# Optimization experiments

Hardware: AMD Instinct MI355X
Metric: run time of the kernel (lower is better)

## Reference

```python
import jax, jax.numpy as jnp
import numpy as np

B, N, DPOS, F, P, K = 32, 1024, 3, 64, 128, 16


def setup_inputs() -> dict:
    key = jax.random.key(0)
    kp, kf, kw1, kw2 = jax.random.split(key, 4)
    points = jax.random.normal(kp, (B, N, DPOS), dtype=jnp.float32)
    features = jax.random.normal(kf, (B, N, F), dtype=jnp.float32)
    W1 = jax.random.normal(kw1, (2 * F, 2 * P), dtype=jnp.float32) * (1.0 / np.sqrt(2 * F))
    b1 = jnp.zeros((2 * P,), dtype=jnp.float32)
    W2 = jax.random.normal(kw2, (2 * P, P), dtype=jnp.float32) * (1.0 / np.sqrt(2 * P))
    b2 = jnp.zeros((P,), dtype=jnp.float32)
    return {"points": points, "features": features, "W1": W1, "b1": b1, "W2": W2, "b2": b2}


def reference(points, features, W1, b1, W2, b2):
    # pairwise squared distances: r_i - 2 p_i.p_j + r_j + 1e-5  -> [B, N, N]
    r = jnp.sum(points * points, axis=2, keepdims=True)
    m = jnp.einsum('bnd,bmd->bnm', points, points)
    D = r - 2.0 * m + jnp.swapaxes(r, 1, 2) + 1e-5
    # K+1 nearest (incl. self), drop self -> indices [B, N, K]
    _, idx = jax.lax.top_k(-D, K + 1)
    idx = idx[:, :, 1:]
    # gather neighbor features: [B, N, K, F]
    neighbors = features[jnp.arange(B)[:, None, None], idx]
    center = jnp.broadcast_to(features[:, :, None, :], neighbors.shape)
    local = jnp.concatenate([neighbors - center, center], axis=-1)  # [B,N,K,2F]
    # 2-layer MLP with exact GELU
    h = jax.nn.gelu(jnp.einsum('bnkf,fh->bnkh', local, W1) + b1, approximate=False)
    out = jax.nn.gelu(jnp.einsum('bnkh,hp->bnkp', h, W2) + b2, approximate=False)
    # mean over neighbors -> [B, N, P]
    return jnp.mean(out, axis=2)
```

## Files before the change

kernel.cpp:

```cpp
#include <hip/hip_runtime.h>
#include <math.h>

#define BB 32
#define NN 1024
#define FF 64
#define PP 128
#define KNN 16
#define H2 256
#define F2 128
#define KSEL 17
#define SVCAP 272

typedef float f32x4 __attribute__((ext_vector_type(4)));
typedef _Float16 f16x8 __attribute__((ext_vector_type(8)));
typedef _Float16 f16x4 __attribute__((ext_vector_type(4)));
typedef _Float16 f16x2 __attribute__((ext_vector_type(2)));

#define GC1 0.39616247f
#define GC3 -0.05891477f
#define GC5 0.00563735f
#define GC7 -2.10439e-4f
#define GXC 3.2988f

__device__ __forceinline__ f16x8 splat8(float f) {
    _Float16 h = (_Float16)f;
    f16x8 v = {h, h, h, h, h, h, h, h};
    return v;
}
__device__ __forceinline__ f16x4 splat4(float f) {
    _Float16 h = (_Float16)f;
    f16x4 v = {h, h, h, h};
    return v;
}

__device__ __forceinline__ f16x8 act8(f16x8 gv, f16x8 qv) {
    const f16x8 XL = splat8(-GXC), XH = splat8(GXC);
    const f16x8 C1 = splat8(GC1), C3 = splat8(GC3), C5 = splat8(GC5), C7 = splat8(GC7);
    const f16x8 HF = splat8(0.5f);
    f16x8 x  = gv + qv;
    f16x8 xc = __builtin_elementwise_min(__builtin_elementwise_max(x, XL), XH);
    f16x8 s  = xc * xc;
    f16x8 t  = s * C7 + C5;
    t = s * t + C3;
    t = s * t + C1;
    f16x8 u = xc * t + HF;
    return x * u;
}

__device__ __forceinline__ float gelu4_sum(f32x4 a, float bias) {
    f16x4 x;
    x[0] = (_Float16)(a[0] + bias);
    x[1] = (_Float16)(a[1] + bias);
    x[2] = (_Float16)(a[2] + bias);
    x[3] = (_Float16)(a[3] + bias);
    const f16x4 XL = splat4(-GXC), XH = splat4(GXC);
    const f16x4 C1 = splat4(GC1), C3 = splat4(GC3), C5 = splat4(GC5), C7 = splat4(GC7);
    const f16x4 HF = splat4(0.5f);
    f16x4 xc = __builtin_elementwise_min(__builtin_elementwise_max(x, XL), XH);
    f16x4 s  = xc * xc;
    f16x4 t  = s * C7 + C5;
    t = s * t + C3;
    t = s * t + C1;
    f16x4 u = xc * t + HF;
    f16x4 y = x * u;
    f16x2 y2 = __builtin_shufflevector(y, y, 0, 1) + __builtin_shufflevector(y, y, 2, 3);
    return (float)y2[0] + (float)y2[1];
}

template <int OFF>
__device__ __forceinline__ f16x8 gload(const char* a) {
    f16x8 d;
    asm volatile("global_load_dwordx4 %0, %1, off offset:%c2"
                 : "=v"(d) : "v"(a), "i"(OFF));
    return d;
}
template <int N>
__device__ __forceinline__ void vwait() {
    asm volatile("s_waitcnt vmcnt(%c0)" ::"i"(N) : "memory");
    __builtin_amdgcn_sched_barrier(0);
}

__global__ __launch_bounds__(512) void prep_weights(const float* __restrict__ W1,
                                                    const float* __restrict__ W2,
                                                    _Float16* __restrict__ Wcf,
                                                    _Float16* __restrict__ W2f) {
    int tid = blockIdx.x * 512 + threadIdx.x;
    if (tid < 4096) {
        const int lane = tid & 63, quad = lane >> 4, l16 = lane & 15;
        const int kk = (tid >> 6) & 1, n_tile = tid >> 7;
        const int n = n_tile * 16 + l16;
        const int kb = kk * 32 + quad * 8;
        f16x8 v;
#pragma unroll
        for (int j = 0; j < 8; ++j) {
            const int k = kb + j;
            float x = (n < 256) ? W1[k * 256 + n]
                                : (W1[(64 + k) * 256 + (n - 256)] - W1[k * 256 + (n - 256)]);
            v[j] = (_Float16)x;
        }
        *(f16x8*)(Wcf + (size_t)tid * 8) = v;
    } else {
        const int t2 = tid - 4096;
        const int lane = t2 & 63, quad = lane >> 4, l16 = lane & 15;
        const int nt = (t2 >> 6) & 7, kk8 = t2 >> 9;
        const int p = nt * 16 + l16;
        const int hb = kk8 * 32 + quad * 8;
        f16x8 v;
#pragma unroll
        for (int j = 0; j < 8; ++j) v[j] = (_Float16)W2[(size_t)(hb + j) * PP + p];
        *(f16x8*)(W2f + (size_t)t2 * 8) = v;
    }
}

__global__ __launch_bounds__(512, 8) void knn_gq(const float* __restrict__ points,
                                                 int* __restrict__ idx_out,
                                                 const float* __restrict__ feat,
                                                 const _Float16* __restrict__ Wcf,
                                                 const float* __restrict__ b1,
                                                 _Float16* __restrict__ Gall,
                                                 _Float16* __restrict__ Qall) {
    __shared__ __align__(16) unsigned char smem[35840];
    const int t = threadIdx.x;

    if (blockIdx.x >= 4096) {
        _Float16 (*st)[16][136] = (_Float16(*)[16][136])smem;
        const int w8 = t >> 6, lane = t & 63;
        const int w4 = w8 & 3;
        const int quad = lane >> 4, l16 = lane & 15;
        const int gb = blockIdx.x - 4096;
        const int m0 = gb * 32 + (w8 >> 2) * 16;

        f16x8 a[2];
#pragma unroll
        for (int kk = 0; kk < 2; ++kk) {
            const float* ap = feat + (size_t)(m0 + l16) * 64 + kk * 32 + quad * 8;
            float4 a0 = *(const float4*)ap, a1 = *(const float4*)(ap + 4);
            f16x8 v;
            v[0] = (_Float16)a0.x; v[1] = (_Float16)a0.y; v[2] = (_Float16)a0.z; v[3] = (_Float16)a0.w;
            v[4] = (_Float16)a1.x; v[5] = (_Float16)a1.y; v[6] = (_Float16)a1.z; v[7] = (_Float16)a1.w;
            a[kk] = v;
        }
        f32x4 acc[8];
#pragma unroll
        for (int nt = 0; nt < 8; ++nt) acc[nt] = (f32x4){0.f, 0.f, 0.f, 0.f};
#pragma unroll
        for (int kk = 0; kk < 2; ++kk)
#pragma unroll
            for (int nt = 0; nt < 8; ++nt) {
                f16x8 bf = *(const f16x8*)(Wcf + (size_t)(((w4 * 8 + nt) * 2 + kk) * 64 + lane) * 8);
                acc[nt] = __builtin_amdgcn_mfma_f32_16x16x32_f16(a[kk], bf, acc[nt], 0, 0, 0);
            }

        const bool isQ = (w4 >= 2);
#pragma unroll
        for (int nt = 0; nt < 8; ++nt) {
            const int col = nt * 16 + l16;
            const float bias = isQ ? b1[(w4 - 2) * 128 + col] : 0.f;
#pragma unroll
            for (int r = 0; r < 4; ++r)
                st[w8][quad * 4 + r][col] = (_Float16)(acc[nt][r] + bias);
        }
        __syncthreads();

        const int row = lane >> 2, c = lane & 3;
        const int m = m0 + row;
#pragma unroll
        for (int i = 0; i < 4; ++i) {
            const int col = c * 32 + i * 8;
            f16x8 v = *(const f16x8*)&st[w8][row][col];
            if (!isQ) *(f16x8*)(Gall + (size_t)m * H2 + w4 * 128 + col) = v;
            else      *(f16x8*)(Qall + (size_t)m * H2 + (w4 - 2) * 128 + col) = v;
        }
        return;
    }

    float2* pxy = (float2*)smem;
    float2* pzr = (float2*)(smem + 8192);
    unsigned (*sv_val)[SVCAP] = (unsigned(*)[SVCAP])(smem + 16384);
    unsigned (*sv_idx)[SVCAP] = (unsigned(*)[SVCAP])(smem + 25088);
    unsigned (*tie_idx)[64]   = (unsigned(*)[64])(smem + 33792);

    const int w = t >> 6, lane = t & 63;
    const int b = blockIdx.x >> 7;
    const int q0 = (blockIdx.x & 127) * 8;
    const float* pb = points + (size_t)b * NN * 3;
    const unsigned long long lt = (1ull << lane) - 1ull;

    for (int i = t; i < NN; i += 512) {
        float x = pb[3 * i], y = pb[3 * i + 1], z = pb[3 * i + 2];
        float r = __fadd_rn(__fadd_rn(__fmul_rn(x, x), __fmul_rn(y, y)), __fmul_rn(z, z));
        pxy[i] = make_float2(x, y);
        pzr[i] = make_float2(z, r);
    }
    __syncthreads();

    const int qn = q0 + w;
    const int gq = b * NN + qn;
    const float2 qv1 = pxy[qn], qv2 = pzr[qn];
    const float qx = qv1.x, qy = qv1.y, qz = qv2.x, qw = qv2.y;

    float D[16];
#pragma unroll
    for (int j = 0; j < 16; ++j) {
        const int m = j * 64 + lane;
        const float2 v1 = pxy[m], v2 = pzr[m];
        float dot = __fadd_rn(__fadd_rn(__fmul_rn(qx, v1.x), __fmul_rn(qy, v1.y)),
                              __fmul_rn(qz, v2.x));
        D[j] = __fadd_rn(__fadd_rn(__fsub_rn(qw, __fmul_rn(2.0f, dot)), v2.y), 1e-5f);
    }

    float mnf = D[0];
#pragma unroll
    for (int j = 1; j < 16; ++j) mnf = fminf(mnf, D[j]);
    const unsigned mbits = __float_as_uint(mnf);

    const unsigned mhi = mbits >> 16;
    unsigned Thi = 0;
#pragma unroll
    for (int bit = 15; bit >= 0; --bit) {
        unsigned cand = Thi | (1u << bit);
        int cnt = __popcll(__ballot(mhi < cand));
        if (cnt < KSEL) Thi = cand;
    }
    const unsigned T = (Thi << 16) | 0xFFFFu;

    unsigned base = 0;
#pragma unroll
    for (int j = 0; j < 16; ++j) {
        unsigned vb = __float_as_uint(D[j]);
        bool keep = (vb <= T);
        unsigned long long m = __ballot(keep);
        if (keep) {
            unsigned pos = base + (unsigned)__popcll(m & lt);
            if (pos < SVCAP) { sv_val[w][pos] = vb; sv_idx[w][pos] = j * 64 + lane; }
        }
        base += (unsigned)__popcll(m);
    }
    unsigned C = base > SVCAP ? SVCAP : base;

    unsigned rv[5], ri[5];
#pragma unroll
    for (int s = 0; s < 5; ++s) {
        int i = s * 64 + lane;
        bool ok = (i < (int)C);
        rv[s] = ok ? sv_val[w][i] : 0xFFFFFFFFu;
        ri[s] = ok ? sv_idx[w][i] : 0xFFFFFFFFu;
    }

    unsigned Ts = 0;
    if (C <= 64) {
#pragma unroll
        for (int bit = 31; bit >= 0; --bit) {
            unsigned cand = Ts | (1u << bit);
            int cnt = __popcll(__ballot(rv[0] < cand));
            if (cnt < KSEL) Ts = cand;
        }
    } else {
#pragma unroll
        for (int bit = 31; bit >= 0; --bit) {
            unsigned cand = Ts | (1u << bit);
            int cnt = 0;
#pragma unroll
            for (int s = 0; s < 5; ++s)
                cnt += __popcll(__ballot(rv[s] < cand));
            if (cnt < KSEL) Ts = cand;
        }
    }

    int L = 0;
#pragma unroll
    for (int s = 0; s < 5; ++s) L += __popcll(__ballot(rv[s] < Ts));
    const int need = KSEL - L;

    unsigned vmin_l = 0xFFFFFFFFu;
#pragma unroll
    for (int s = 0; s < 5; ++s) vmin_l = vmin_l < rv[s] ? vmin_l : rv[s];
#pragma unroll
    for (int off = 32; off >= 1; off >>= 1) {
        unsigned o2 = __shfl_xor(vmin_l, off, 64);
        vmin_l = vmin_l < o2 ? vmin_l : o2;
    }
    const unsigned Vmin = vmin_l;
    unsigned imin_l = 0xFFFFFFFFu;
#pragma unroll
    for (int s = 0; s < 5; ++s)
        if (rv[s] == Vmin && ri[s] < imin_l) imin_l = ri[s];
#pragma unroll
    for (int off = 32; off >= 1; off >>= 1) {
        unsigned o2 = __shfl_xor(imin_l, off, 64);
        imin_l = imin_l < o2 ? imin_l : o2;
    }
    const unsigned dropIdx = imin_l;

    int* o = idx_out + (size_t)gq * KNN;
    unsigned wbase = 0, tbase = 0;
#pragma unroll
    for (int s = 0; s < 5; ++s) {
        unsigned vb = rv[s], mi = ri[s];
        bool wk = (vb < Ts) && (mi != dropIdx);
        unsigned long long wm = __ballot(wk);
        if (wk) o[wbase + (unsigned)__popcll(wm & lt)] = (int)mi;
        wbase += (unsigned)__popcll(wm);
        bool tk = (vb == Ts);
        unsigned long long tm2 = __ballot(tk);
        if (tk) {
            unsigned tp = tbase + (unsigned)__popcll(tm2 & lt);
            if (tp < 64) tie_idx[w][tp] = mi;
        }
        tbase += (unsigned)__popcll(tm2);
    }
    unsigned tc = tbase > 64 ? 64 : tbase;
    if ((int)tc == need) {
        bool tk = (lane < (int)tc);
        unsigned mi2 = tk ? tie_idx[w][lane] : 0xFFFFFFFFu;
        tk = tk && (mi2 != dropIdx);
        unsigned long long m3 = __ballot(tk);
        if (tk) o[wbase + (unsigned)__popcll(m3 & lt)] = (int)mi2;
    } else if (lane == 0) {
        unsigned pos = wbase;
        for (int r = 0; r < need; ++r) {
            unsigned best = 0xFFFFFFFFu; int bj = 0;
            for (int j2 = 0; j2 < (int)tc; ++j2) {
                unsigned mi = tie_idx[w][j2];
                if (mi < best) { best = mi; bj = j2; }
            }
            tie_idx[w][bj] = 0xFFFFFFFFu;
            if (best != dropIdx) o[pos++] = (int)best;
        }
    }
}

__global__ __launch_bounds__(512, 3) void fused_mlp14(const _Float16* __restrict__ Gall,
                                                      const _Float16* __restrict__ Qall,
                                                      const int* __restrict__ knn_idx,
                                                      const _Float16* __restrict__ W2f,
                                                      const float* __restrict__ b2,
                                                      float* __restrict__ out) {
    __shared__ __align__(16) _Float16 w2s[32768];
    const int t = threadIdx.x, w = t >> 6, lane = t & 63;
    const int quad = lane >> 4, l16 = lane & 15;

    const int lb = ((blockIdx.x & 7) << 8) | (blockIdx.x >> 3);

    const int q0 = lb * 16 + w * 2;
    const int b = q0 >> 10;
    const int nb0 = knn_idx[q0 * KNN + l16];
    const int nb1 = knn_idx[(q0 + 1) * KNN + l16];
    const _Float16* g0 = Gall + ((size_t)(b << 10) + nb0) * H2;
    const _Float16* g1 = Gall + ((size_t)(b << 10) + nb1) * H2;
    const _Float16* qq0 = Qall + (size_t)q0 * H2;
    const _Float16* qq1 = qq0 + H2;

    const char* aG0 = (const char*)g0 + quad * 16;
    const char* aG1 = (const char*)g1 + quad * 16;
    const char* aQ0 = (const char*)qq0 + quad * 16;
    const char* aQ1 = (const char*)qq1 + quad * 16;

    float bias[8];
#pragma unroll
    for (int nt = 0; nt < 8; ++nt) bias[nt] = b2[nt * 16 + l16];
#pragma unroll
    for (int nt = 0; nt < 8; ++nt) asm volatile("" ::"v"(bias[nt]));

#pragma unroll
    for (int i = 0; i < 8; ++i) {
        f16x8 v = *(const f16x8*)(W2f + (size_t)(i * 4096 + t * 8));
        *(f16x8*)&w2s[i * 4096 + t * 8] = v;
    }

    f32x4 acc[2][8];
#pragma unroll
    for (int tm = 0; tm < 2; ++tm)
#pragma unroll
        for (int nt = 0; nt < 8; ++nt) acc[tm][nt] = (f32x4){0.f, 0.f, 0.f, 0.f};

    __syncthreads();

    f16x8 GA[3], GB[3], QA[3], QB[3];
    GA[0] = gload<0>(aG0);  GB[0] = gload<0>(aG1);
    QA[0] = gload<0>(aQ0);  QB[0] = gload<0>(aQ1);
    GA[1] = gload<64>(aG0); GB[1] = gload<64>(aG1);
    QA[1] = gload<64>(aQ0); QB[1] = gload<64>(aQ1);

#define STEP(RK)                                                                  \
    {                                                                             \
        if ((RK) < 6) {                                                           \
            GA[((RK) + 2) % 3] = gload<((RK) + 2) * 64>(aG0);                     \
            GB[((RK) + 2) % 3] = gload<((RK) + 2) * 64>(aG1);                     \
            QA[((RK) + 2) % 3] = gload<((RK) + 2) * 64>(aQ0);                     \
            QB[((RK) + 2) % 3] = gload<((RK) + 2) * 64>(aQ1);                     \
        }                                                                         \
        vwait<((RK) <= 5 ? 8 : ((RK) == 6 ? 4 : 0))>();                           \
        f16x8 a0 = act8(GA[(RK) % 3], QA[(RK) % 3]);                              \
        f16x8 a1 = act8(GB[(RK) % 3], QB[(RK) % 3]);                              \
        const _Float16* bb = &w2s[(RK) * 4096 + lane * 8];                        \
        _Pragma("unroll")                                                         \
        for (int nt = 0; nt < 8; ++nt) {                                          \
            f16x8 bf = *(const f16x8*)(bb + nt * 512);                            \
            acc[0][nt] = __builtin_amdgcn_mfma_f32_16x16x32_f16(a0, bf, acc[0][nt], 0, 0, 0); \
            acc[1][nt] = __builtin_amdgcn_mfma_f32_16x16x32_f16(a1, bf, acc[1][nt], 0, 0, 0); \
        }                                                                         \
    }
    STEP(0) STEP(1) STEP(2) STEP(3) STEP(4) STEP(5) STEP(6) STEP(7)
#undef STEP

    __syncthreads();
    float* obuf = (float*)w2s;
#pragma unroll
    for (int tm = 0; tm < 2; ++tm)
#pragma unroll
        for (int nt = 0; nt < 8; ++nt) {
            float s = gelu4_sum(acc[tm][nt], bias[nt]);
            s += __shfl_xor(s, 16, 64);
            s += __shfl_xor(s, 32, 64);
            if (quad == 0)
                obuf[(w * 2 + tm) * 128 + nt * 16 + l16] = s * 0.0625f;
        }
    __syncthreads();
    {
        float4 v = *(const float4*)&obuf[t * 4];
        *(float4*)(out + (size_t)lb * 2048 + t * 4) = v;
    }
}

extern "C" void kernel_launch(void* const* d_in, const int* in_sizes, int n_in,
                              void* d_out, int out_size, void* d_ws, size_t ws_size,
                              hipStream_t stream) {
    const float* points   = (const float*)d_in[0];
    const float* features = (const float*)d_in[1];
    const float* W1 = (const float*)d_in[2];
    const float* b1 = (const float*)d_in[3];
    const float* W2 = (const float*)d_in[4];
    const float* b2 = (const float*)d_in[5];
    float* out = (float*)d_out;

    const size_t IDX_B  = (size_t)BB * NN * KNN * 4;
    const size_t WCF_B  = 512 * 64 * 2;
    const size_t W2F_B  = 256 * 128 * 2;
    const size_t G_B    = (size_t)BB * NN * H2 * 2;

    int* knn_idx = (int*)d_ws;
    char* p = (char*)d_ws + IDX_B;
    _Float16* Wcf  = (_Float16*)p;  p += WCF_B;
    _Float16* W2f  = (_Float16*)p;  p += W2F_B;
    _Float16* Gall = (_Float16*)p;  p += G_B;
    _Float16* Qall = (_Float16*)p;

    prep_weights<<<16, 512, 0, stream>>>(W1, W2, Wcf, W2f);
    knn_gq<<<5120, 512, 0, stream>>>(points, knn_idx, features, Wcf, b1, Gall, Qall);
    fused_mlp14<<<2048, 512, 0, stream>>>(Gall, Qall, knn_idx, W2f, b2, out);
}
```

Before: 202.9 us.

## Swizzle block-to-data mapping and replace asm prefetch pipeline with compiler-scheduled loads

The knn and G/Q projection blocks now remap blockIdx so that consecutive blocks spread across batches and row groups, which likely aims at better cache or XCD locality. In the MLP kernel, the hand-written inline-asm triple-buffered global loads with explicit vmcnt waits are removed. Instead, the first two k-steps are issued before the shared-memory weight copy and the rest load plainly, leaving scheduling to the compiler. s_setprio is raised around the MFMA bursts so that waves doing math get priority. The risk is that the compiler hoists loads less aggressively, which exposes latency, and that the remapping may hurt L2 reuse.

```diff
diff --git a/kernel.cpp b/kernel.cpp
--- a/kernel.cpp
+++ b/kernel.cpp
@@ -67,19 +67,6 @@
     return (float)y2[0] + (float)y2[1];
 }
 
-template <int OFF>
-__device__ __forceinline__ f16x8 gload(const char* a) {
-    f16x8 d;
-    asm volatile("global_load_dwordx4 %0, %1, off offset:%c2"
-                 : "=v"(d) : "v"(a), "i"(OFF));
-    return d;
-}
-template <int N>
-__device__ __forceinline__ void vwait() {
-    asm volatile("s_waitcnt vmcnt(%c0)" ::"i"(N) : "memory");
-    __builtin_amdgcn_sched_barrier(0);
-}
-
 __global__ __launch_bounds__(512) void prep_weights(const float* __restrict__ W1,
                                                     const float* __restrict__ W2,
                                                     _Float16* __restrict__ Wcf,
@@ -128,7 +115,8 @@
         const int w4 = w8 & 3;
         const int quad = lane >> 4, l16 = lane & 15;
         const int gb = blockIdx.x - 4096;
-        const int m0 = gb * 32 + (w8 >> 2) * 16;
+        const int gbl = ((gb & 7) << 7) | (gb >> 3);
+        const int m0 = gbl * 32 + (w8 >> 2) * 16;
 
         f16x8 a[2];
 #pragma unroll
@@ -180,9 +168,11 @@
     unsigned (*sv_idx)[SVCAP] = (unsigned(*)[SVCAP])(smem + 25088);
     unsigned (*tie_idx)[64]   = (unsigned(*)[64])(smem + 33792);
 
+    const int lbk = ((blockIdx.x & 7) << 9) | (blockIdx.x >> 3);
+
     const int w = t >> 6, lane = t & 63;
-    const int b = blockIdx.x >> 7;
-    const int q0 = (blockIdx.x & 127) * 8;
+    const int b = lbk >> 7;
+    const int q0 = (lbk & 127) * 8;
     const float* pb = points + (size_t)b * NN * 3;
     const unsigned long long lt = (1ull << lane) - 1ull;
 
@@ -330,7 +320,7 @@
     }
 }
 
-__global__ __launch_bounds__(512, 3) void fused_mlp14(const _Float16* __restrict__ Gall,
+__global__ __launch_bounds__(512, 3) void fused_mlp15(const _Float16* __restrict__ Gall,
                                                       const _Float16* __restrict__ Qall,
                                                       const int* __restrict__ knn_idx,
                                                       const _Float16* __restrict__ W2f,
@@ -351,16 +341,19 @@
     const _Float16* qq0 = Qall + (size_t)q0 * H2;
     const _Float16* qq1 = qq0 + H2;
 
-    const char* aG0 = (const char*)g0 + quad * 16;
-    const char* aG1 = (const char*)g1 + quad * 16;
-    const char* aQ0 = (const char*)qq0 + quad * 16;
-    const char* aQ1 = (const char*)qq1 + quad * 16;
-
     float bias[8];
 #pragma unroll
     for (int nt = 0; nt < 8; ++nt) bias[nt] = b2[nt * 16 + l16];
-#pragma unroll
-    for (int nt = 0; nt < 8; ++nt) asm volatile("" ::"v"(bias[nt]));
+
+    const int h0 = quad * 8, h1 = 32 + quad * 8;
+    f16x8 p0gA = *(const f16x8*)(g0 + h0);
+    f16x8 p0qA = *(const f16x8*)(qq0 + h0);
+    f16x8 p0gB = *(const f16x8*)(g1 + h0);
+    f16x8 p0qB = *(const f16x8*)(qq1 + h0);
+    f16x8 p1gA = *(const f16x8*)(g0 + h1);
+    f16x8 p1qA = *(const f16x8*)(qq0 + h1);
+    f16x8 p1gB = *(const f16x8*)(g1 + h1);
+    f16x8 p1qB = *(const f16x8*)(qq1 + h1);
 
 #pragma unroll
     for (int i = 0; i < 8; ++i) {
@@ -376,33 +369,36 @@
 
     __syncthreads();
 
-    f16x8 GA[3], GB[3], QA[3], QB[3];
-    GA[0] = gload<0>(aG0);  GB[0] = gload<0>(aG1);
-    QA[0] = gload<0>(aQ0);  QB[0] = gload<0>(aQ1);
-    GA[1] = gload<64>(aG0); GB[1] = gload<64>(aG1);
-    QA[1] = gload<64>(aQ0); QB[1] = gload<64>(aQ1);
-
-#define STEP(RK)                                                                  \
-    {                                                                             \
-        if ((RK) < 6) {                                                           \
-            GA[((RK) + 2) % 3] = gload<((RK) + 2) * 64>(aG0);                     \
-            GB[((RK) + 2) % 3] = gload<((RK) + 2) * 64>(aG1);                     \
-            QA[((RK) + 2) % 3] = gload<((RK) + 2) * 64>(aQ0);                     \
-            QB[((RK) + 2) % 3] = gload<((RK) + 2) * 64>(aQ1);                     \
-        }                                                                         \
-        vwait<((RK) <= 5 ? 8 : ((RK) == 6 ? 4 : 0))>();                           \
-        f16x8 a0 = act8(GA[(RK) % 3], QA[(RK) % 3]);                              \
-        f16x8 a1 = act8(GB[(RK) % 3], QB[(RK) % 3]);                              \
-        const _Float16* bb = &w2s[(RK) * 4096 + lane * 8];                        \
-        _Pragma("unroll")                                                         \
-        for (int nt = 0; nt < 8; ++nt) {                                          \
-            f16x8 bf = *(const f16x8*)(bb + nt * 512);                            \
+#define BODY(RK, GA_, QA_, GB_, QB_)                                                   \
+    {                                                                                  \
+        f16x8 a0 = act8(GA_, QA_);                                                     \
+        f16x8 a1 = act8(GB_, QB_);                                                     \
+        const _Float16* bb = &w2s[(RK) * 4096 + lane * 8];                             \
+        __builtin_amdgcn_s_setprio(1);                                                 \
+        _Pragma("unroll")                                                              \
+        for (int nt = 0; nt < 8; ++nt) {                                               \
+            f16x8 bf = *(const f16x8*)(bb + nt * 512);                                 \
             acc[0][nt] = __builtin_amdgcn_mfma_f32_16x16x32_f16(a0, bf, acc[0][nt], 0, 0, 0); \
             acc[1][nt] = __builtin_amdgcn_mfma_f32_16x16x32_f16(a1, bf, acc[1][nt], 0, 0, 0); \
-        }                                                                         \
-    }
-    STEP(0) STEP(1) STEP(2) STEP(3) STEP(4) STEP(5) STEP(6) STEP(7)
-#undef STEP
+        }                                                                              \
+        __builtin_amdgcn_s_setprio(0);                                                 \
+    }
+
+    BODY(0, p0gA, p0qA, p0gB, p0qB)
+    BODY(1, p1gA, p1qA, p1gB, p1qB)
+
+#define STEPL(RK)                                                                      \
+    {                                                                                  \
+        const int ho = (RK) * 32 + quad * 8;                                           \
+        f16x8 gA = *(const f16x8*)(g0 + ho);                                           \
+        f16x8 qA = *(const f16x8*)(qq0 + ho);                                          \
+        f16x8 gB = *(const f16x8*)(g1 + ho);                                           \
+        f16x8 qB = *(const f16x8*)(qq1 + ho);                                          \
+        BODY(RK, gA, qA, gB, qB)                                                       \
+    }
+    STEPL(2) STEPL(3) STEPL(4) STEPL(5) STEPL(6) STEPL(7)
+#undef STEPL
+#undef BODY
 
     __syncthreads();
     float* obuf = (float*)w2s;
@@ -448,5 +444,5 @@
 
     prep_weights<<<16, 512, 0, stream>>>(W1, W2, Wcf, W2f);
     knn_gq<<<5120, 512, 0, stream>>>(points, knn_idx, features, Wcf, b1, Gall, Qall);
-    fused_mlp14<<<2048, 512, 0, stream>>>(Gall, Qall, knn_idx, W2f, b2, out);
-}
+    fused_mlp15<<<2048, 512, 0, stream>>>(Gall, Qall, knn_idx, W2f, b2, out);
+}
```

Result: faster. 185.2 us (-8.7%).
